# Optimization experiments

Hardware: AMD Instinct MI355X
Metric: run time of the kernel (lower is better)

## Reference

```python
import jax, jax.numpy as jnp
import numpy as np

B, T, TF = 4, 16000, 80
NC, NR, NS, NO, NIN, NL = 80, 64, 256, 256, 256, 16
K_UP, STRIDE = 800, 200
LOOP_FACTOR = 8  # floor(log2(128)) + 1


def setup_inputs() -> dict:
    key = jax.random.key(0)
    ks = jax.random.split(key, 16)
    s = 0.05
    return {
        "features": jax.random.normal(ks[0], (B, NC, TF), jnp.float32),
        "forward_input": jax.random.randint(ks[1], (B, T), 0, NIN, jnp.int32),
        "embed_table": jax.random.normal(ks[2], (NIN, NR), jnp.float32) * s,
        "up_w": jax.random.normal(ks[3], (NC, NC, K_UP), jnp.float32) * s,  # torch ConvTranspose1d (in,out,K)
        "up_b": jnp.zeros((NC,), jnp.float32),
        "cond_w": jax.random.normal(ks[4], (2 * NR * NL, NC), jnp.float32) * s,
        "cond_b": jnp.zeros((2 * NR * NL,), jnp.float32),
        "dil_w": jax.random.normal(ks[5], (NL, 2 * NR, NR, 2), jnp.float32) * s,
        "dil_b": jnp.zeros((NL, 2 * NR), jnp.float32),
        "res_w": jax.random.normal(ks[6], (NL - 1, NR, NR), jnp.float32) * s,
        "res_b": jnp.zeros((NL - 1, NR), jnp.float32),
        "skip_w": jax.random.normal(ks[7], (NL, NS, NR), jnp.float32) * s,
        "skip_b": jnp.zeros((NL, NS), jnp.float32),
        "out_w": jax.random.normal(ks[8], (NO, NS), jnp.float32) * s,
        "end_w": jax.random.normal(ks[9], (NO, NO), jnp.float32) * s,
    }


def reference(features, forward_input, embed_table, up_w, up_b, cond_w, cond_b,
              dil_w, dil_b, res_w, res_b, skip_w, skip_b, out_w, end_w):
    # ConvTranspose1d(stride=200): conv with lhs_dilation, spatially-flipped kernel, in/out swapped
    k_t = jnp.flip(up_w, -1).transpose(1, 0, 2)  # (out, in, K)
    cond = jax.lax.conv_general_dilated(
        features, k_t, window_strides=(1,), padding=[(K_UP - 1, K_UP - 1)],
        lhs_dilation=(STRIDE,), dimension_numbers=('NCH', 'OIH', 'NCH'))
    cond = cond + up_b[None, :, None]
    cond = cond[:, :, :T]  # truncate to signal length

    x = embed_table[forward_input].transpose(0, 2, 1)  # [B, NR, T]

    cond_acts = jnp.einsum('oc,bct->bot', cond_w, cond) + cond_b[None, :, None]
    cond_acts = cond_acts.reshape(B, NL, 2 * NR, T)

    res_acts = None
    output = None
    for i in range(NL):
        d = 2 ** (i % LOOP_FACTOR)
        prev = jnp.pad(x, ((0, 0), (0, 0), (d, 0)))[:, :, :T]  # causal shift by dilation
        in_act = (jnp.einsum('oi,bit->bot', dil_w[i, :, :, 0], prev)
                  + jnp.einsum('oi,bit->bot', dil_w[i, :, :, 1], x)
                  + dil_b[i][None, :, None] + cond_acts[:, i])
        acts = jnp.tanh(in_act[:, :NR]) * jax.nn.sigmoid(in_act[:, NR:])
        if i < NL - 1:
            res_acts = jnp.einsum('oi,bit->bot', res_w[i], acts) + res_b[i][None, :, None]
        # NOTE: faithful to original: on last layer res_acts is stale (from layer NL-2)
        x = res_acts + x
        skip = jnp.einsum('oi,bit->bot', skip_w[i], acts) + skip_b[i][None, :, None]
        output = skip if output is None else output + skip

    output = jax.nn.relu(output)
    output = jax.nn.relu(jnp.einsum('os,bst->bot', out_w, output))
    output = jnp.einsum('oi,bit->bot', end_w, output)
    # shift right by one, zero-fill first frame
    output = jnp.concatenate([jnp.zeros_like(output[:, :, :1]), output[:, :, :-1]], axis=2)
    return output
```

## Files before the change

kernel.cpp:

```cpp
#include <hip/hip_runtime.h>
#include <hip/hip_bf16.h>

#define TT 16000
#define BB 4
#define NLAYER 16
#define NBLK 1000
#define BARSTR 1088
#define BARSZ (15 * BARSTR)
#define XCSTR 72
#define XPSTR 72
#define ACSTR 72
#define CDSTR 88
#define M3STR 264
#define ABSTR 72

#define A1SZ (NLAYER*8*7*512)
#define A2SZ (NLAYER*4*2*512)
#define SWSZ (16*32*512)
#define OWSZ (16*8*512)
#define AUPSZ (20*10*512)
#define BUPSZ (1000*10*512)

typedef unsigned short ushort_t;
typedef unsigned long long u64_t;
typedef short v8s __attribute__((ext_vector_type(8)));
typedef short v4s __attribute__((ext_vector_type(4)));
typedef float v4f __attribute__((ext_vector_type(4)));

#define MFMA16 __builtin_amdgcn_mfma_f32_16x16x32_bf16

__device__ __forceinline__ float bf2f(ushort_t u) {
  unsigned int x = ((unsigned int)u) << 16;
  float f; __builtin_memcpy(&f, &x, 4); return f;
}
__device__ __forceinline__ ushort_t f2bf(float f) {
  unsigned int x; __builtin_memcpy(&x, &f, 4);
  x += 0x7fffu + ((x >> 16) & 1u);
  return (ushort_t)(x >> 16);
}

__global__ __launch_bounds__(256) void kprep(
    const float* __restrict__ feat, const int* __restrict__ fin,
    const float* __restrict__ embed, const float* __restrict__ up_w,
    const float* __restrict__ cond_w, const float* __restrict__ cond_b,
    const float* __restrict__ dil_w, const float* __restrict__ dil_b,
    const float* __restrict__ res_w, const float* __restrict__ skip_w,
    const float* __restrict__ skip_b, const float* __restrict__ out_w,
    const float* __restrict__ end_w,
    ushort_t* __restrict__ A1, ushort_t* __restrict__ A2,
    ushort_t* __restrict__ SWf, ushort_t* __restrict__ OWf,
    ushort_t* __restrict__ EWf, ushort_t* __restrict__ Aup,
    ushort_t* __restrict__ Bup, ushort_t* __restrict__ x0,
    float* __restrict__ Bcomb, float* __restrict__ SBsum,
    unsigned int* __restrict__ bar) {
  int tid = blockIdx.x * 256 + threadIdx.x;
  int np = gridDim.x * 256;
  for (int idx = tid; idx < BARSZ; idx += np) bar[idx] = 0u;
  for (int idx = tid; idx < A1SZ; idx += np) {
    int j = idx & 7, lane = (idx >> 3) & 63;
    int r_ = idx >> 9;
    int ks = r_ % 7; int r2 = r_ / 7;
    int mt = r2 & 7; int i = r2 >> 3;
    int m = mt * 16 + (lane & 15);
    int k = ks * 32 + (lane >> 4) * 8 + j;
    float v = 0.f;
    if (k < 64)       v = dil_w[((i * 128 + m) * 64 + k) * 2 + 1];
    else if (k < 128) v = dil_w[((i * 128 + m) * 64 + (k - 64)) * 2 + 0];
    else if (k < 208) v = cond_w[(i * 128 + m) * 80 + (k - 128)];
    A1[idx] = f2bf(v);
  }
  for (int idx = tid; idx < A2SZ; idx += np) {
    int j = idx & 7, lane = (idx >> 3) & 63;
    int r_ = idx >> 9;
    int ks = r_ & 1; int mt = (r_ >> 1) & 3; int i = r_ >> 3;
    int m = mt * 16 + (lane & 15);
    int k = ks * 32 + (lane >> 4) * 8 + j;
    A2[idx] = f2bf(i < 15 ? res_w[(i * 64 + m) * 64 + k] : 0.f);
  }
  for (int idx = tid; idx < SWSZ; idx += np) {
    int j = idx & 7, lane = (idx >> 3) & 63;
    int r_ = idx >> 9;
    int ks = r_ & 31; int mt = r_ >> 5;
    int m = mt * 16 + (lane & 15);
    int k = ks * 32 + (lane >> 4) * 8 + j;
    int i = k >> 6, ch = k & 63;
    SWf[idx] = f2bf(skip_w[(i * 256 + m) * 64 + ch]);
  }
  for (int idx = tid; idx < OWSZ; idx += np) {
    int j = idx & 7, lane = (idx >> 3) & 63;
    int r_ = idx >> 9;
    int ks = r_ & 7; int mt = r_ >> 3;
    int m = mt * 16 + (lane & 15);
    int k = ks * 32 + (lane >> 4) * 8 + j;
    OWf[idx] = f2bf(out_w[m * 256 + k]);
    EWf[idx] = f2bf(end_w[m * 256 + k]);
  }
  for (int idx = tid; idx < AUPSZ; idx += np) {
    int j = idx & 7, lane = (idx >> 3) & 63;
    int r_ = idx >> 9;
    int ks = r_ % 10; int mt = r_ / 10;
    int mrow = mt * 16 + (lane & 15);
    int km = ks * 32 + (lane >> 4) * 8 + j;
    int b = mrow / 80, q = mrow % 80;
    int m = km / 80, i = km % 80;
    int jj = q - m;
    Aup[idx] = f2bf(jj >= 0 ? feat[(b * 80 + i) * 80 + jj] : 0.f);
  }
  for (size_t idx = tid; idx < (size_t)80 * 80 * 800; idx += np) {
    int kk = (int)(idx % 800); int io = (int)(idx / 800);
    int o = io % 80, i = io / 80;
    int m = kk / 200, r = kk - m * 200;
    int col = o * 200 + r;
    int nt = col >> 4, tl = col & 15;
    int km = m * 80 + i;
    int ks = km >> 5, j = km & 7;
    int lane = (((km >> 3) & 3) << 4) | tl;
    Bup[(((size_t)nt * 10 + ks) * 64 + lane) * 8 + j] = f2bf(up_w[idx]);
  }
  for (int idx = tid; idx < BB * TT * 64; idx += np) {
    int k = idx & 63;
    int bt = idx >> 6;
    x0[idx] = f2bf(embed[fin[bt] * 64 + k]);
  }
  for (int idx = tid; idx < NLAYER * 128; idx += np)
    Bcomb[idx] = dil_b[idx] + cond_b[idx];
  for (int idx = tid; idx < 256; idx += np) {
    float s = 0.f;
    for (int i = 0; i < NLAYER; i++) s += skip_b[i * 256 + idx];
    SBsum[idx] = s;
  }
}

__global__ __launch_bounds__(256) void kup(
    const ushort_t* __restrict__ Aup, const ushort_t* __restrict__ Bup,
    const float* __restrict__ up_b, ushort_t* __restrict__ cond) {
  int nt0 = blockIdx.x * 4;
  int lane = threadIdx.x & 63;
  int w = threadIdx.x >> 6;
  int tl = lane & 15, quad = lane >> 4;
  v4f acc[5][4];
  #pragma unroll
  for (int mt = 0; mt < 5; mt++)
    #pragma unroll
    for (int nt = 0; nt < 4; nt++) acc[mt][nt] = 0.f;
  #pragma unroll
  for (int ks = 0; ks < 10; ks++) {
    v8s bf[4];
    #pragma unroll
    for (int nt = 0; nt < 4; nt++)
      bf[nt] = *(const v8s*)(Bup + (((size_t)(nt0 + nt) * 10 + ks) * 64 + lane) * 8);
    #pragma unroll
    for (int mt = 0; mt < 5; mt++) {
      v8s a = *(const v8s*)(Aup + (((size_t)(w * 5 + mt) * 10 + ks) * 64 + lane) * 8);
      #pragma unroll
      for (int nt = 0; nt < 4; nt++)
        acc[mt][nt] = MFMA16(a, bf[nt], acc[mt][nt], 0, 0, 0);
    }
  }
  #pragma unroll
  for (int mt = 0; mt < 5; mt++) {
    #pragma unroll
    for (int nt = 0; nt < 4; nt++) {
      int col = (nt0 + nt) * 16 + tl;
      int o = col / 200, r = col % 200;
      float bias = up_b[o];
      #pragma unroll
      for (int rg = 0; rg < 4; rg++) {
        int mrow = (w * 5 + mt) * 16 + quad * 4 + rg;
        int b = mrow / 80, q = mrow % 80;
        cond[((size_t)b * TT + q * 200 + r) * 80 + o] = f2bf(acc[mt][nt][rg] + bias);
      }
    }
  }
}

__global__ __launch_bounds__(256, 4) void kchain(
    ushort_t* __restrict__ x0g, ushort_t* __restrict__ x1g,
    const ushort_t* __restrict__ cond, ushort_t* __restrict__ actsb,
    const ushort_t* __restrict__ A1, const ushort_t* __restrict__ A2,
    const float* __restrict__ Bcomb, const float* __restrict__ resb,
    unsigned int* __restrict__ bar) {
  __shared__ ushort_t Uxc[64 * XCSTR];
  __shared__ ushort_t Uhalo[64 * XPSTR];
  __shared__ ushort_t Uact[64 * ACSTR];
  __shared__ ushort_t Ucd[64 * CDSTR + 8];
  int b = blockIdx.y;
  int t0 = blockIdx.x * 64;
  int tidx = threadIdx.x;
  int lane = tidx & 63;
  int w = tidx >> 6;
  int tl = lane & 15, quad = lane >> 4;
  int cha = w * 16 + quad * 4;
  const size_t lstr = (size_t)BB * TT * 64;

  const ushort_t* xb0 = x0g + ((size_t)b * TT + t0) * 64;
  for (int e = tidx * 8; e < 4096; e += 2048) {
    int t = e >> 6, c = e & 63;
    *(v8s*)&Uxc[t * XCSTR + c] = *(const v8s*)(xb0 + e);
  }
  const ushort_t* cbp = cond + ((size_t)b * TT + t0) * 80;
  for (int e = tidx * 8; e < 5120; e += 2048) {
    int t = e / 80, c = e - t * 80;
    *(v8s*)&Ucd[t * CDSTR + c] = *(const v8s*)(cbp + e);
  }
  for (int e2 = tidx; e2 < 520; e2 += 256) {
    if (e2 < 512) Ucd[(e2 >> 3) * CDSTR + 80 + (e2 & 7)] = 0;
    else          Ucd[64 * CDSTR + (e2 - 512)] = 0;
  }
  __syncthreads();

  for (int l = 0; l < NLAYER; l++) {
    int d = 1 << (l & 7);
    int hr = (d < 64) ? d : 64;
    const ushort_t* xing = (l & 1) ? x1g : x0g;
    ushort_t* xoutg = (l & 1) ? x0g : x1g;
    const ushort_t* A1l = A1 + (size_t)l * 8 * 7 * 512;
    const ushort_t* A2l = A2 + (size_t)l * 4 * 2 * 512;
    const float* Bb = Bcomb + l * 128;
    const float* rb = resb + (l < 15 ? l : 0) * 64;
    int last = (l == NLAYER - 1);

    for (int e = tidx * 8; e < hr * 64; e += 2048) {
      int t = e >> 6, c = e & 63;
      int tp = t0 + t - d;
      v8s v = (v8s)0;
      if (tp >= 0) {
        const u64_t* p = (const u64_t*)(xing + ((size_t)b * TT + tp) * 64 + c);
        u64_t w0 = __hip_atomic_load(p, __ATOMIC_RELAXED, __HIP_MEMORY_SCOPE_AGENT);
        u64_t w1 = __hip_atomic_load(p + 1, __ATOMIC_RELAXED, __HIP_MEMORY_SCOPE_AGENT);
        __builtin_memcpy(&v, &w0, 8);
        __builtin_memcpy(((char*)&v) + 8, &w1, 8);
      }
      *(v8s*)&Uhalo[t * XPSTR + c] = v;
    }
    __syncthreads();

    v4f acc0[4], acc1[4];
    #pragma unroll
    for (int nt = 0; nt < 4; nt++) { acc0[nt] = 0.f; acc1[nt] = 0.f; }
    #pragma unroll
    for (int ks = 0; ks < 7; ks++) {
      v8s a0 = *(const v8s*)(A1l + (((size_t)w * 7 + ks) * 64 + lane) * 8);
      v8s a1 = *(const v8s*)(A1l + (((size_t)(w + 4) * 7 + ks) * 64 + lane) * 8);
      #pragma unroll
      for (int nt = 0; nt < 4; nt++) {
        int t = nt * 16 + tl;
        const ushort_t* bp;
        if (ks < 2) {
          bp = &Uxc[t * XCSTR + ks * 32 + quad * 8];
        } else if (ks < 4) {
          int toff = t - d;
          bp = (toff >= 0) ? &Uxc[toff * XCSTR + (ks - 2) * 32 + quad * 8]
                           : &Uhalo[t * XPSTR + (ks - 2) * 32 + quad * 8];
        } else {
          bp = &Ucd[t * CDSTR + (ks - 4) * 32 + quad * 8];
        }
        v8s bf = *(const v8s*)bp;
        acc0[nt] = MFMA16(a0, bf, acc0[nt], 0, 0, 0);
        acc1[nt] = MFMA16(a1, bf, acc1[nt], 0, 0, 0);
      }
    }

    float ba[4], bb_[4];
    #pragma unroll
    for (int r = 0; r < 4; r++) { ba[r] = Bb[cha + r]; bb_[r] = Bb[64 + cha + r]; }
    #pragma unroll
    for (int nt = 0; nt < 4; nt++) {
      int t = nt * 16 + tl;
      v4s pk;
      #pragma unroll
      for (int r = 0; r < 4; r++) {
        float ia = acc0[nt][r] + ba[r];
        float ib = acc1[nt][r] + bb_[r];
        float ax = fabsf(ia);
        float e2 = __expf(-2.f * ax);
        float th = __builtin_copysignf((1.f - e2) / (1.f + e2), ia);
        float sg = 1.f / (1.f + __expf(-ib));
        pk[r] = (short)f2bf(th * sg);
      }
      *(v4s*)&Uact[t * ACSTR + cha] = pk;
    }
    __syncthreads();

    ushort_t* ab = actsb + (size_t)l * lstr + ((size_t)b * TT + t0) * 64;
    for (int e = tidx * 8; e < 4096; e += 2048) {
      int t = e >> 6, c = e & 63;
      *(v8s*)(ab + e) = *(const v8s*)&Uact[t * ACSTR + c];
    }

    if (!last) {
      v4f acc2[4];
      #pragma unroll
      for (int nt = 0; nt < 4; nt++) {
        v4f z;
        #pragma unroll
        for (int r = 0; r < 4; r++) z[r] = rb[cha + r];
        acc2[nt] = z;
      }
      #pragma unroll
      for (int ks = 0; ks < 2; ks++) {
        v8s a = *(const v8s*)(A2l + (((size_t)w * 2 + ks) * 64 + lane) * 8);
        #pragma unroll
        for (int nt = 0; nt < 4; nt++) {
          v8s bf = *(const v8s*)&Uact[(nt * 16 + tl) * ACSTR + ks * 32 + quad * 8];
          acc2[nt] = MFMA16(a, bf, acc2[nt], 0, 0, 0);
        }
      }
      #pragma unroll
      for (int nt = 0; nt < 4; nt++) {
        int t = nt * 16 + tl;
        v4s xo = *(const v4s*)&Uxc[t * XCSTR + cha];
        v4s nw;
        #pragma unroll
        for (int r = 0; r < 4; r++)
          nw[r] = (short)f2bf(acc2[nt][r] + bf2f((ushort_t)xo[r]));
        *(v4s*)&Uxc[t * XCSTR + cha] = nw;
      }
      __syncthreads();

      int dnext = 1 << ((l + 1) & 7);
      int tmin = 64 - (dnext < 64 ? dnext : 64);
      ushort_t* xob = xoutg + ((size_t)b * TT + t0) * 64;
      for (int e = tidx * 8; e < 4096; e += 2048) {
        int t = e >> 6, c = e & 63;
        if (t >= tmin) {
          v8s v = *(const v8s*)&Uxc[t * XCSTR + c];
          u64_t w0, w1;
          __builtin_memcpy(&w0, &v, 8);
          __builtin_memcpy(&w1, ((const char*)&v) + 8, 8);
          u64_t* p = (u64_t*)(xob + e);
          __hip_atomic_store(p, w0, __ATOMIC_RELAXED, __HIP_MEMORY_SCOPE_AGENT);
          __hip_atomic_store(p + 1, w1, __ATOMIC_RELAXED, __HIP_MEMORY_SCOPE_AGENT);
        }
      }

      __syncthreads();
      if (tidx == 0) {
        unsigned int* L = bar + l * BARSTR;
        int flat = b * 250 + blockIdx.x;
        int shard = flat & 15;
        unsigned int tgt = (shard < 8) ? 62u : 61u;
        unsigned int old = __hip_atomic_fetch_add(L + shard * 32, 1u,
            __ATOMIC_RELAXED, __HIP_MEMORY_SCOPE_AGENT);
        if (old == tgt) {
          unsigned int ro = __hip_atomic_fetch_add(L + 16 * 32, 1u,
              __ATOMIC_RELAXED, __HIP_MEMORY_SCOPE_AGENT);
          if (ro == 15u) {
            #pragma unroll
            for (int s = 0; s < 16; s++)
              __hip_atomic_store(L + (17 + s) * 32, 1u,
                  __ATOMIC_RELAXED, __HIP_MEMORY_SCOPE_AGENT);
          }
        }
        while (__hip_atomic_load(L + (17 + shard) * 32,
            __ATOMIC_RELAXED, __HIP_MEMORY_SCOPE_AGENT) == 0u)
          __builtin_amdgcn_s_sleep(16);
      }
      __syncthreads();
    }
  }
}

__global__ __launch_bounds__(256) void kfinal(
    const ushort_t* __restrict__ actsb,
    const ushort_t* __restrict__ SWf, const ushort_t* __restrict__ OWf,
    const ushort_t* __restrict__ EWf, const float* __restrict__ SBsum,
    float* __restrict__ dout) {
  __shared__ ushort_t SMEM[64 * M3STR];
  int b = blockIdx.y;
  int t0 = blockIdx.x * 64;
  int tidx = threadIdx.x;
  int lane = tidx & 63;
  int w = tidx >> 6;
  int tl = lane & 15, quad = lane >> 4;

  v4f acc[4][4];
  #pragma unroll
  for (int mt = 0; mt < 4; mt++) {
    int o = (w * 4 + mt) * 16 + quad * 4;
    #pragma unroll
    for (int nt = 0; nt < 4; nt++) {
      v4f z;
      #pragma unroll
      for (int r = 0; r < 4; r++) z[r] = SBsum[o + r];
      acc[mt][nt] = z;
    }
  }
  const ushort_t* abase = actsb + ((size_t)b * TT + t0) * 64;
  const size_t lstr = (size_t)BB * TT * 64;
  int tq = tidx >> 2;
  int pq = (tidx & 3) * 16;
  {
    const ushort_t* a0 = abase + tq * 64 + pq;
    v8s p0 = *(const v8s*)(a0);
    v8s p1 = *(const v8s*)(a0 + 8);
    *(v8s*)&SMEM[tq * ABSTR + pq] = p0;
    *(v8s*)&SMEM[tq * ABSTR + pq + 8] = p1;
  }
  __syncthreads();
  for (int l = 0; l < NLAYER; l++) {
    int ln = (l + 1 < NLAYER) ? (l + 1) : (NLAYER - 1);
    const ushort_t* an = abase + (size_t)ln * lstr + tq * 64 + pq;
    v8s q0 = *(const v8s*)(an);
    v8s q1 = *(const v8s*)(an + 8);
    const ushort_t* ABc = SMEM + (l & 1) * (64 * ABSTR);
    #pragma unroll
    for (int ks2 = 0; ks2 < 2; ks2++) {
      int ksg = l * 2 + ks2;
      v8s bf[4];
      #pragma unroll
      for (int nt = 0; nt < 4; nt++)
        bf[nt] = *(const v8s*)&ABc[(nt * 16 + tl) * ABSTR + ks2 * 32 + quad * 8];
      #pragma unroll
      for (int mt = 0; mt < 4; mt++) {
        v8s a = *(const v8s*)(SWf + (((size_t)(w * 4 + mt) * 32 + ksg) * 64 + lane) * 8);
        #pragma unroll
        for (int nt = 0; nt < 4; nt++)
          acc[mt][nt] = MFMA16(a, bf[nt], acc[mt][nt], 0, 0, 0);
      }
    }
    ushort_t* ABn = SMEM + ((l + 1) & 1) * (64 * ABSTR);
    *(v8s*)&ABn[tq * ABSTR + pq] = q0;
    *(v8s*)&ABn[tq * ABSTR + pq + 8] = q1;
    __syncthreads();
  }
  #pragma unroll
  for (int mt = 0; mt < 4; mt++) {
    int o = (w * 4 + mt) * 16 + quad * 4;
    #pragma unroll
    for (int nt = 0; nt < 4; nt++) {
      int t = nt * 16 + tl;
      #pragma unroll
      for (int r = 0; r < 4; r++)
        SMEM[t * M3STR + o + r] = f2bf(fmaxf(acc[mt][nt][r], 0.f));
    }
  }
  __syncthreads();

  v4f acc2[4][4];
  #pragma unroll
  for (int mt = 0; mt < 4; mt++)
    #pragma unroll
    for (int nt = 0; nt < 4; nt++) acc2[mt][nt] = 0.f;
  #pragma unroll
  for (int ks = 0; ks < 8; ks++) {
    v8s bf[4];
    #pragma unroll
    for (int nt = 0; nt < 4; nt++)
      bf[nt] = *(const v8s*)&SMEM[(nt * 16 + tl) * M3STR + ks * 32 + quad * 8];
    #pragma unroll
    for (int mt = 0; mt < 4; mt++) {
      v8s a = *(const v8s*)(OWf + (((size_t)(w * 4 + mt) * 8 + ks) * 64 + lane) * 8);
      #pragma unroll
      for (int nt = 0; nt < 4; nt++)
        acc2[mt][nt] = MFMA16(a, bf[nt], acc2[mt][nt], 0, 0, 0);
    }
  }
  __syncthreads();
  #pragma unroll
  for (int mt = 0; mt < 4; mt++) {
    int o = (w * 4 + mt) * 16 + quad * 4;
    #pragma unroll
    for (int nt = 0; nt < 4; nt++) {
      int t = nt * 16 + tl;
      #pragma unroll
      for (int r = 0; r < 4; r++)
        SMEM[t * M3STR + o + r] = f2bf(fmaxf(acc2[mt][nt][r], 0.f));
    }
  }
  __syncthreads();

  v4f acc3[4][4];
  #pragma unroll
  for (int mt = 0; mt < 4; mt++)
    #pragma unroll
    for (int nt = 0; nt < 4; nt++) acc3[mt][nt] = 0.f;
  #pragma unroll
  for (int ks = 0; ks < 8; ks++) {
    v8s bf[4];
    #pragma unroll
    for (int nt = 0; nt < 4; nt++)
      bf[nt] = *(const v8s*)&SMEM[(nt * 16 + tl) * M3STR + ks * 32 + quad * 8];
    #pragma unroll
    for (int mt = 0; mt < 4; mt++) {
      v8s a = *(const v8s*)(EWf + (((size_t)(w * 4 + mt) * 8 + ks) * 64 + lane) * 8);
      #pragma unroll
      for (int nt = 0; nt < 4; nt++)
        acc3[mt][nt] = MFMA16(a, bf[nt], acc3[mt][nt], 0, 0, 0);
    }
  }
  #pragma unroll
  for (int mt = 0; mt < 4; mt++) {
    #pragma unroll
    for (int nt = 0; nt < 4; nt++) {
      int tg = t0 + nt * 16 + tl;
      #pragma unroll
      for (int r = 0; r < 4; r++) {
        int o = (w * 4 + mt) * 16 + quad * 4 + r;
        float* ob = dout + ((size_t)b * 256 + o) * TT;
        if (tg == 0) ob[0] = 0.f;
        if (tg + 1 < TT) ob[tg + 1] = acc3[mt][nt][r];
      }
    }
  }
}

extern "C" void kernel_launch(void* const* d_in, const int* in_sizes, int n_in,
                              void* d_out, int out_size, void* d_ws, size_t ws_size,
                              hipStream_t stream) {
  const float* feat   = (const float*)d_in[0];
  const int*   fin    = (const int*)d_in[1];
  const float* embed  = (const float*)d_in[2];
  const float* up_w   = (const float*)d_in[3];
  const float* up_b   = (const float*)d_in[4];
  const float* cond_w = (const float*)d_in[5];
  const float* cond_b = (const float*)d_in[6];
  const float* dil_w  = (const float*)d_in[7];
  const float* dil_b  = (const float*)d_in[8];
  const float* res_w  = (const float*)d_in[9];
  const float* res_b  = (const float*)d_in[10];
  const float* skip_w = (const float*)d_in[11];
  const float* skip_b = (const float*)d_in[12];
  const float* out_w  = (const float*)d_in[13];
  const float* end_w  = (const float*)d_in[14];

  float* ws = (float*)d_ws;
  unsigned int* bar = (unsigned int*)ws;
  size_t off = BARSZ;
  float* Bcomb = ws + off; off += NLAYER * 128;
  float* SBsum = ws + off; off += 256;
  ushort_t* ub = (ushort_t*)(ws + off);
  size_t uo = 0;
  ushort_t* A1   = ub + uo; uo += A1SZ;
  ushort_t* A2   = ub + uo; uo += A2SZ;
  ushort_t* SWf  = ub + uo; uo += SWSZ;
  ushort_t* OWf  = ub + uo; uo += OWSZ;
  ushort_t* EWf  = ub + uo; uo += OWSZ;
  ushort_t* Aup  = ub + uo; uo += AUPSZ;
  ushort_t* Bup  = ub + uo; uo += BUPSZ;
  ushort_t* cond = ub + uo; uo += (size_t)BB * TT * 80;
  ushort_t* x0   = ub + uo; uo += (size_t)BB * TT * 64;
  ushort_t* x1   = ub + uo; uo += (size_t)BB * TT * 64;
  ushort_t* acts = ub + uo; uo += (size_t)NLAYER * BB * TT * 64;

  kprep<<<1024, 256, 0, stream>>>(feat, fin, embed, up_w, cond_w, cond_b,
      dil_w, dil_b, res_w, skip_w, skip_b, out_w, end_w,
      A1, A2, SWf, OWf, EWf, Aup, Bup, x0, Bcomb, SBsum, bar);
  kup<<<250, 256, 0, stream>>>(Aup, Bup, up_b, cond);
  kchain<<<dim3(250, BB), 256, 0, stream>>>(x0, x1, cond, acts,
      A1, A2, Bcomb, res_b, bar);
  kfinal<<<dim3(250, BB), 256, 0, stream>>>(acts, SWf, OWf, EWf, SBsum,
      (float*)d_out);
}
```

Measured before the change: 467.1 us.

## Deepen kfinal activation prefetch to two layers and coalesce Bup weight repack

Measured after the change: 431.4 us. 7.7% less time.

```diff
diff --git a/kernel.cpp b/kernel.cpp
--- a/kernel.cpp
+++ b/kernel.cpp
@@ -106,16 +106,15 @@
     int jj = q - m;
     Aup[idx] = f2bf(jj >= 0 ? feat[(b * 80 + i) * 80 + jj] : 0.f);
   }
-  for (size_t idx = tid; idx < (size_t)80 * 80 * 800; idx += np) {
-    int kk = (int)(idx % 800); int io = (int)(idx / 800);
-    int o = io % 80, i = io / 80;
-    int m = kk / 200, r = kk - m * 200;
-    int col = o * 200 + r;
-    int nt = col >> 4, tl = col & 15;
-    int km = m * 80 + i;
-    int ks = km >> 5, j = km & 7;
-    int lane = (((km >> 3) & 3) << 4) | tl;
-    Bup[(((size_t)nt * 10 + ks) * 64 + lane) * 8 + j] = f2bf(up_w[idx]);
+  for (int idx = tid; idx < BUPSZ; idx += np) {
+    int j = idx & 7, lane = (idx >> 3) & 63;
+    int r_ = idx >> 9;
+    int ks = r_ % 10; int nt = r_ / 10;
+    int km = ks * 32 + (lane >> 4) * 8 + j;
+    int m = km / 80, i = km % 80;
+    int col = nt * 16 + (lane & 15);
+    int o = col / 200, r = col % 200;
+    Bup[idx] = f2bf(up_w[(size_t)(i * 80 + o) * 800 + m * 200 + r]);
   }
   for (int idx = tid; idx < BB * TT * 64; idx += np) {
     int k = idx & 63;
@@ -361,6 +360,27 @@
   }
 }
 
+#define KF_COMPUTE(L, BUF)                                                    \
+  {                                                                           \
+    _Pragma("unroll")                                                         \
+    for (int ks2 = 0; ks2 < 2; ks2++) {                                       \
+      int ksg = (L) * 2 + ks2;                                                \
+      v8s bf[4];                                                              \
+      _Pragma("unroll")                                                       \
+      for (int nt = 0; nt < 4; nt++)                                          \
+        bf[nt] = *(const v8s*)&(BUF)[(nt * 16 + tl) * ABSTR + ks2 * 32 +      \
+                                     quad * 8];                               \
+      _Pragma("unroll")                                                       \
+      for (int mt = 0; mt < 4; mt++) {                                        \
+        v8s a = *(const v8s*)(SWf +                                           \
+            (((size_t)(w * 4 + mt) * 32 + ksg) * 64 + lane) * 8);             \
+        _Pragma("unroll")                                                     \
+        for (int nt = 0; nt < 4; nt++)                                        \
+          acc[mt][nt] = MFMA16(a, bf[nt], acc[mt][nt], 0, 0, 0);              \
+      }                                                                       \
+    }                                                                         \
+  }
+
 __global__ __launch_bounds__(256) void kfinal(
     const ushort_t* __restrict__ actsb,
     const ushort_t* __restrict__ SWf, const ushort_t* __restrict__ OWf,
@@ -386,42 +406,39 @@
       acc[mt][nt] = z;
     }
   }
-  const ushort_t* abase = actsb + ((size_t)b * TT + t0) * 64;
   const size_t lstr = (size_t)BB * TT * 64;
   int tq = tidx >> 2;
   int pq = (tidx & 3) * 16;
+  const ushort_t* a0p = actsb + ((size_t)b * TT + t0) * 64 + tq * 64 + pq;
   {
-    const ushort_t* a0 = abase + tq * 64 + pq;
-    v8s p0 = *(const v8s*)(a0);
-    v8s p1 = *(const v8s*)(a0 + 8);
+    v8s p0 = *(const v8s*)(a0p);
+    v8s p1 = *(const v8s*)(a0p + 8);
     *(v8s*)&SMEM[tq * ABSTR + pq] = p0;
     *(v8s*)&SMEM[tq * ABSTR + pq + 8] = p1;
   }
+  v8s qa0 = *(const v8s*)(a0p + 1 * lstr);
+  v8s qa1 = *(const v8s*)(a0p + 1 * lstr + 8);
+  v8s qb0 = *(const v8s*)(a0p + 2 * lstr);
+  v8s qb1 = *(const v8s*)(a0p + 2 * lstr + 8);
   __syncthreads();
-  for (int l = 0; l < NLAYER; l++) {
-    int ln = (l + 1 < NLAYER) ? (l + 1) : (NLAYER - 1);
-    const ushort_t* an = abase + (size_t)ln * lstr + tq * 64 + pq;
-    v8s q0 = *(const v8s*)(an);
-    v8s q1 = *(const v8s*)(an + 8);
-    const ushort_t* ABc = SMEM + (l & 1) * (64 * ABSTR);
-    #pragma unroll
-    for (int ks2 = 0; ks2 < 2; ks2++) {
-      int ksg = l * 2 + ks2;
-      v8s bf[4];
-      #pragma unroll
-      for (int nt = 0; nt < 4; nt++)
-        bf[nt] = *(const v8s*)&ABc[(nt * 16 + tl) * ABSTR + ks2 * 32 + quad * 8];
-      #pragma unroll
-      for (int mt = 0; mt < 4; mt++) {
-        v8s a = *(const v8s*)(SWf + (((size_t)(w * 4 + mt) * 32 + ksg) * 64 + lane) * 8);
-        #pragma unroll
-        for (int nt = 0; nt < 4; nt++)
-          acc[mt][nt] = MFMA16(a, bf[nt], acc[mt][nt], 0, 0, 0);
-      }
-    }
-    ushort_t* ABn = SMEM + ((l + 1) & 1) * (64 * ABSTR);
-    *(v8s*)&ABn[tq * ABSTR + pq] = q0;
-    *(v8s*)&ABn[tq * ABSTR + pq + 8] = q1;
+  for (int l = 0; l < NLAYER; l += 2) {
+    KF_COMPUTE(l, SMEM);
+    *(v8s*)&SMEM[64 * ABSTR + tq * ABSTR + pq] = qa0;
+    *(v8s*)&SMEM[64 * ABSTR + tq * ABSTR + pq + 8] = qa1;
+    {
+      int ln = (l + 3 < NLAYER) ? (l + 3) : (NLAYER - 1);
+      qa0 = *(const v8s*)(a0p + (size_t)ln * lstr);
+      qa1 = *(const v8s*)(a0p + (size_t)ln * lstr + 8);
+    }
+    __syncthreads();
+    KF_COMPUTE(l + 1, SMEM + 64 * ABSTR);
+    *(v8s*)&SMEM[tq * ABSTR + pq] = qb0;
+    *(v8s*)&SMEM[tq * ABSTR + pq + 8] = qb1;
+    {
+      int ln = (l + 4 < NLAYER) ? (l + 4) : (NLAYER - 1);
+      qb0 = *(const v8s*)(a0p + (size_t)ln * lstr);
+      qb1 = *(const v8s*)(a0p + (size_t)ln * lstr + 8);
+    }
     __syncthreads();
   }
   #pragma unroll
```
